# Optimization experiments

Measured on AMD Instinct MI355X. Metric: run time of the kernel, lower is better.

The kernel has to match this reference:

```python
import jax, jax.numpy as jnp
import numpy as np

# RT-DETR multi-scale deformable attention reference (PPMSDeformableAttention forward, value_mask=None)
SPATIAL_SHAPES = ((80, 80), (40, 40), (20, 20))  # (H, W) per level; sum(H*W) = 8400 = Len_v
NUM_HEADS = 8
NUM_LEVELS = 3
NUM_POINTS = 4


def _gather_corner(v_l, ix, iy, H, W):
    # v_l: [bs, heads, H*W, hd]; ix/iy: [bs, heads, N] int32 pixel indices (possibly out of range)
    valid = (ix >= 0) & (ix < W) & (iy >= 0) & (iy < H)
    idx = jnp.clip(iy, 0, H - 1) * W + jnp.clip(ix, 0, W - 1)
    g = jnp.take_along_axis(v_l, idx[..., None], axis=2)  # [bs, heads, N, hd]
    return jnp.where(valid[..., None], g, jnp.zeros((), v_l.dtype))


def _bilinear_sample(v_l, px, py, H, W):
    # grid_sample(align_corners=False, padding_mode='zeros') semantics.
    # v_l: [bs, heads, H*W, hd]; px/py: [bs, heads, N] continuous pixel coords
    x0 = jnp.floor(px).astype(jnp.int32)
    y0 = jnp.floor(py).astype(jnp.int32)
    x1, y1 = x0 + 1, y0 + 1
    wx1 = px - x0.astype(px.dtype)
    wy1 = py - y0.astype(py.dtype)
    wx0, wy0 = 1.0 - wx1, 1.0 - wy1
    out = (_gather_corner(v_l, x0, y0, H, W) * (wx0 * wy0)[..., None]
           + _gather_corner(v_l, x1, y0, H, W) * (wx1 * wy0)[..., None]
           + _gather_corner(v_l, x0, y1, H, W) * (wx0 * wy1)[..., None]
           + _gather_corner(v_l, x1, y1, H, W) * (wx1 * wy1)[..., None])
    return out  # [bs, heads, N, hd]


def setup_inputs() -> dict:
    key = jax.random.key(0)
    ks = jax.random.split(key, 8)
    bs, Lq, C = 32, 300, 256
    Lv = sum(h * w for h, w in SPATIAL_SHAPES)
    tp = NUM_HEADS * NUM_LEVELS * NUM_POINTS  # 96
    s = 1.0 / np.sqrt(C)
    return {
        "query": jax.random.normal(ks[0], (bs, Lq, C), jnp.float32),
        "reference_points": jax.random.uniform(ks[1], (bs, Lq, NUM_LEVELS, 4), jnp.float32, 0.05, 0.95),
        "value": jax.random.normal(ks[2], (bs, Lv, C), jnp.float32),
        "Wv": jax.random.normal(ks[3], (C, C), jnp.float32) * s,
        "bv": jnp.zeros((C,), jnp.float32),
        "Woff": jax.random.normal(ks[4], (C, tp * 2), jnp.float32) * (s * 0.1),
        "boff": jax.random.normal(ks[5], (tp * 2,), jnp.float32) * 0.5,
        "Watt": jax.random.normal(ks[6], (C, tp), jnp.float32) * s,
        "batt": jnp.zeros((tp,), jnp.float32),
        "Wout": jax.random.normal(ks[7], (C, C), jnp.float32) * s,
        "bout": jnp.zeros((C,), jnp.float32),
    }


def reference(query, reference_points, value, Wv, bv, Woff, boff, Watt, batt, Wout, bout):
    bs, Lq, C = query.shape
    H_, L, P = NUM_HEADS, NUM_LEVELS, NUM_POINTS
    hd = C // H_
    Lv = value.shape[1]

    # value projection -> [bs, heads, Lv, hd]
    v = (value @ Wv + bv).reshape(bs, Lv, H_, hd).transpose(0, 2, 1, 3)

    # sampling offsets and attention weights from query
    off = (query @ Woff + boff).reshape(bs, Lq, H_, L, P, 2)
    attw = jax.nn.softmax((query @ Watt + batt).reshape(bs, Lq, H_, L * P), axis=-1)
    attw = attw.reshape(bs, Lq, H_, L, P)

    # reference_points last dim == 4: (cx, cy, w, h) normalized
    ref_xy = reference_points[:, :, None, :, None, :2]  # [bs,Lq,1,L,1,2]
    ref_wh = reference_points[:, :, None, :, None, 2:]
    loc = ref_xy + off / P * ref_wh * 0.5  # [bs,Lq,H,L,P,2], normalized [0,1]

    out = jnp.zeros((bs, Lq, H_, hd), query.dtype)
    start = 0
    for l, (H, W) in enumerate(SPATIAL_SHAPES):
        v_l = v[:, :, start:start + H * W]  # [bs, heads, H*W, hd]
        start += H * W
        # normalized -> pixel coords (align_corners=False): p = loc * size - 0.5
        locl = loc[:, :, :, l]  # [bs, Lq, heads, P, 2]
        px = locl[..., 0] * W - 0.5
        py = locl[..., 1] * H - 0.5
        # [bs, Lq, heads, P] -> [bs, heads, Lq*P]
        px = px.transpose(0, 2, 1, 3).reshape(bs, H_, Lq * P)
        py = py.transpose(0, 2, 1, 3).reshape(bs, H_, Lq * P)
        sampled = _bilinear_sample(v_l, px, py, H, W)  # [bs, heads, Lq*P, hd]
        sampled = sampled.reshape(bs, H_, Lq, P, hd)
        out = out + jnp.einsum('bhqpd,bqhp->bqhd', sampled, attw[:, :, :, l])

    out = out.reshape(bs, Lq, C)
    return out @ Wout + bout
```

## Files before the change

### kernel.cpp

```cpp
#include <hip/hip_runtime.h>
#include <hip/hip_bf16.h>

#define BS 32
#define LQ 300
#define CDIM 256
#define HEADS 8
#define HD 32
#define NLEVELS 3
#define NPOINTS 4
#define LV 8400
#define NOA 288

typedef __attribute__((ext_vector_type(4))) float f32x4;
typedef __attribute__((ext_vector_type(8))) short short8;
typedef __attribute__((ext_vector_type(8))) unsigned short u16x8;
typedef __attribute__((ext_vector_type(4))) unsigned short u16x4;

__device__ __forceinline__ unsigned short f2bf(float f) {
    __hip_bfloat16 h = __float2bfloat16(f);
    return __bfloat16_as_ushort(h);
}
__device__ __forceinline__ float bf2f(unsigned short u) {
    union { unsigned u; float f; } v; v.u = ((unsigned)u) << 16;
    return v.f;
}

__global__ void prep_weights_kernel(
    const float* __restrict__ Wv, const float* __restrict__ Wout,
    const float* __restrict__ Woff, const float* __restrict__ Watt,
    unsigned short* __restrict__ WvT, unsigned short* __restrict__ WoutT,
    unsigned short* __restrict__ WoaT)
{
    const int bid = blockIdx.x;
    const int k = threadIdx.x;
    if (bid < 256) {
        WvT[bid * 256 + k] = f2bf(Wv[k * 256 + bid]);
    } else if (bid < 512) {
        const int n = bid - 256;
        WoutT[n * 256 + k] = f2bf(Wout[k * 256 + n]);
    } else {
        const int n = bid - 512;
        const float w = (n < 192) ? Woff[k * 192 + n] : Watt[k * 96 + (n - 192)];
        WoaT[n * 256 + k] = f2bf(w);
    }
}

#define BM 128
#define BK 32
#define PAD 40
#define EPAD 264
#define NT (CDIM / BK)

__global__ __launch_bounds__(512) void proj_value_mfma(
    const float* __restrict__ value, const unsigned short* __restrict__ WvT,
    const float* __restrict__ bv, unsigned short* __restrict__ vout)
{
    __shared__ alignas(16) unsigned short lds_w[2][256 * PAD];
    __shared__ alignas(16) unsigned short lds_x[2][128 * PAD];
    unsigned short* lds_ep = &lds_w[0][0];

    const int tid = threadIdx.x;
    const int lane = tid & 63;
    const int wave = tid >> 6;
    const int wm = wave >> 2;
    const int wn = wave & 3;
    const long row0 = (long)blockIdx.x * BM;

    const int wr = tid >> 1, wk = (tid & 1) * 16;
    const unsigned short* wptr = WvT + (size_t)wr * CDIM + wk;
    const int xr = tid >> 2, xk = (tid & 3) * 8;
    const float* xptr = value + (row0 + xr) * CDIM + xk;

    u16x8 wA0, wA1, wB0, wB1;
    f32x4 xA0, xA1, xB0, xB1;

#define LOADSET(s, kb) do {                                   \
        const u16x8* qw_ = (const u16x8*)(wptr + (kb));       \
        w##s##0 = qw_[0]; w##s##1 = qw_[1];                   \
        const float* p_ = xptr + (kb);                        \
        x##s##0 = *(const f32x4*)(p_);                        \
        x##s##1 = *(const f32x4*)(p_ + 4);                    \
    } while (0)

#define WRITESET(s, buf) do {                                 \
        u16x8* ww_ = (u16x8*)&lds_w[buf][wr * PAD + wk];      \
        ww_[0] = w##s##0; ww_[1] = w##s##1;                   \
        u16x8 t_;                                             \
        t_[0] = f2bf(x##s##0[0]); t_[1] = f2bf(x##s##0[1]);   \
        t_[2] = f2bf(x##s##0[2]); t_[3] = f2bf(x##s##0[3]);   \
        t_[4] = f2bf(x##s##1[0]); t_[5] = f2bf(x##s##1[1]);   \
        t_[6] = f2bf(x##s##1[2]); t_[7] = f2bf(x##s##1[3]);   \
        *(u16x8*)&lds_x[buf][xr * PAD + xk] = t_;             \
    } while (0)

    f32x4 acc[4][4] = {};
    const int la = lane & 15;
    const int lg = lane >> 4;

#define COMPUTE(buf) do {                                                     \
        const unsigned short* pw_ = &lds_w[buf][(wn * 64 + la) * PAD + lg * 8];\
        const unsigned short* px_ = &lds_x[buf][(wm * 64 + la) * PAD + lg * 8];\
        short8 xf_[4];                                                        \
        _Pragma("unroll")                                                     \
        for (int mf = 0; mf < 4; ++mf)                                        \
            xf_[mf] = *(const short8*)(px_ + mf * 16 * PAD);                  \
        _Pragma("unroll")                                                     \
        for (int nf = 0; nf < 4; ++nf) {                                      \
            const short8 wf_ = *(const short8*)(pw_ + nf * 16 * PAD);         \
            _Pragma("unroll")                                                 \
            for (int mf = 0; mf < 4; ++mf)                                    \
                acc[nf][mf] = __builtin_amdgcn_mfma_f32_16x16x32_bf16(        \
                    wf_, xf_[mf], acc[nf][mf], 0, 0, 0);                      \
        }                                                                     \
    } while (0)

    LOADSET(A, 0);
    LOADSET(B, BK);
    WRITESET(A, 0);
    __syncthreads();

#pragma unroll
    for (int t = 0; t < NT; t += 2) {
        WRITESET(B, 1);
        if (t + 2 < NT) LOADSET(A, (t + 2) * BK);
        COMPUTE(0);
        __syncthreads();
        if (t + 2 < NT) WRITESET(A, 0);
        if (t + 3 < NT) LOADSET(B, (t + 3) * BK);
        COMPUTE(1);
        __syncthreads();
    }

#pragma unroll
    for (int pass = 0; pass < 2; ++pass) {
        __syncthreads();
        if (wm == pass) {
#pragma unroll
            for (int nf = 0; nf < 4; ++nf) {
                const int nbase = wn * 64 + nf * 16 + lg * 4;
                const f32x4 bb = *(const f32x4*)&bv[nbase];
#pragma unroll
                for (int mf = 0; mf < 4; ++mf) {
                    const int mloc = mf * 16 + la;
                    u16x4 o;
#pragma unroll
                    for (int j = 0; j < 4; ++j) o[j] = f2bf(acc[nf][mf][j] + bb[j]);
                    *(u16x4*)&lds_ep[mloc * EPAD + nbase] = o;
                }
            }
        }
        __syncthreads();
        const int er = tid >> 3;
        const int ec = (tid & 7) * 32;
        const long gr = row0 + pass * 64 + er;
        const u16x8* src = (const u16x8*)&lds_ep[er * EPAD + ec];
        u16x8* dst = (u16x8*)&vout[gr * CDIM + ec];
#pragma unroll
        for (int i = 0; i < 4; ++i) dst[i] = src[i];
    }
#undef LOADSET
#undef WRITESET
#undef COMPUTE
}

#define APAD 40
#define BPAD 40

__global__ __launch_bounds__(256) void offatt_gemm_mfma(
    const float* __restrict__ query, const unsigned short* __restrict__ WoaT,
    const float* __restrict__ boff, const float* __restrict__ batt,
    float* __restrict__ offatt)
{
    __shared__ unsigned short lds_a[2][BM * APAD];
    __shared__ unsigned short lds_b[2][NOA * BPAD];

    const int tid = threadIdx.x;
    const int lane = tid & 63;
    const int wave = tid >> 6;
    const int wm = wave >> 1;
    const int wn = wave & 1;
    const long row0 = (long)blockIdx.x * BM;

    const int ar = tid >> 1;
    const int ak = (tid & 1) * 16;
    const float* aptr = query + (row0 + ar) * CDIM + ak;
    const unsigned short* bptr  = WoaT + (size_t)tid * CDIM;
    const unsigned short* bptr2 = WoaT + (size_t)(256 + tid) * CDIM;
    const bool extra = tid < 32;

    f32x4 arg[4];
    u16x8 brg[4], brg2[4];

    auto load_tile = [&](int kb) {
        const float* p = aptr + kb;
        arg[0] = *(const f32x4*)(p);
        arg[1] = *(const f32x4*)(p + 4);
        arg[2] = *(const f32x4*)(p + 8);
        arg[3] = *(const f32x4*)(p + 12);
        const u16x8* q = (const u16x8*)(bptr + kb);
        brg[0] = q[0]; brg[1] = q[1]; brg[2] = q[2]; brg[3] = q[3];
        if (extra) {
            const u16x8* q2 = (const u16x8*)(bptr2 + kb);
            brg2[0] = q2[0]; brg2[1] = q2[1]; brg2[2] = q2[2]; brg2[3] = q2[3];
        }
    };
    auto write_tile = [&](int buf) {
        u16x8 t0, t1;
#pragma unroll
        for (int i = 0; i < 4; ++i) {
            t0[i]     = f2bf(arg[0][i]);
            t0[i + 4] = f2bf(arg[1][i]);
            t1[i]     = f2bf(arg[2][i]);
            t1[i + 4] = f2bf(arg[3][i]);
        }
        u16x8* wa = (u16x8*)&lds_a[buf][ar * APAD + ak];
        wa[0] = t0; wa[1] = t1;
        u16x8* wb = (u16x8*)&lds_b[buf][tid * BPAD];
        wb[0] = brg[0]; wb[1] = brg[1]; wb[2] = brg[2]; wb[3] = brg[3];
        if (extra) {
            u16x8* wb2 = (u16x8*)&lds_b[buf][(256 + tid) * BPAD];
            wb2[0] = brg2[0]; wb2[1] = brg2[1]; wb2[2] = brg2[2]; wb2[3] = brg2[3];
        }
    };

    f32x4 acc[4][9] = {};
    const int la = lane & 15;
    const int lg = lane >> 4;

    load_tile(0);
    write_tile(0);
    __syncthreads();
    int cur = 0;

    for (int t = 0; t < CDIM / BK; ++t) {
        if (t + 1 < CDIM / BK) load_tile((t + 1) * BK);

        const unsigned short* pa = &lds_a[cur][(wm * 64 + la) * APAD + lg * 8];
        const unsigned short* pb = &lds_b[cur][(wn * 144 + la) * BPAD + lg * 8];
        short8 af[4];
#pragma unroll
        for (int mi = 0; mi < 4; ++mi)
            af[mi] = *(const short8*)(pa + mi * 16 * APAD);
#pragma unroll
        for (int ni = 0; ni < 9; ++ni) {
            const short8 bf = *(const short8*)(pb + ni * 16 * BPAD);
#pragma unroll
            for (int mi = 0; mi < 4; ++mi)
                acc[mi][ni] = __builtin_amdgcn_mfma_f32_16x16x32_bf16(af[mi], bf, acc[mi][ni], 0, 0, 0);
        }

        if (t + 1 < CDIM / BK) write_tile(cur ^ 1);
        __syncthreads();
        cur ^= 1;
    }

    float bias[9];
#pragma unroll
    for (int ni = 0; ni < 9; ++ni) {
        const int col = wn * 144 + ni * 16 + la;
        bias[ni] = (col < 192) ? boff[col] : batt[col - 192];
    }
#pragma unroll
    for (int mi = 0; mi < 4; ++mi) {
#pragma unroll
        for (int ni = 0; ni < 9; ++ni) {
            const int col = wn * 144 + ni * 16 + la;
#pragma unroll
            for (int j = 0; j < 4; ++j) {
                const long r = row0 + wm * 64 + mi * 16 + lg * 4 + j;
                offatt[r * NOA + col] = acc[mi][ni][j] + bias[ni];
            }
        }
    }
}

__global__ __launch_bounds__(256) void sample_kernel(
    const float* __restrict__ offatt, const float* __restrict__ refpts,
    const unsigned short* __restrict__ v, unsigned short* __restrict__ mid)
{
    __shared__ float oa_s[NOA];
    __shared__ float aw_s[96];
    __shared__ float px_s[96];
    __shared__ float py_s[96];

    const int tid = threadIdx.x;
    const int b = blockIdx.x / LQ;
    const int q = blockIdx.x % LQ;
    const long bq = (long)b * LQ + q;

    oa_s[tid] = offatt[bq * NOA + tid];
    if (tid < 32) oa_s[256 + tid] = offatt[bq * NOA + 256 + tid];
    __syncthreads();

    if (tid < 8) {
        float m = -1e30f;
#pragma unroll
        for (int i = 0; i < 12; ++i) m = fmaxf(m, oa_s[192 + tid * 12 + i]);
        float e[12];
        float s = 0.f;
#pragma unroll
        for (int i = 0; i < 12; ++i) { e[i] = __expf(oa_s[192 + tid * 12 + i] - m); s += e[i]; }
        const float inv = 1.f / s;
#pragma unroll
        for (int i = 0; i < 12; ++i) aw_s[tid * 12 + i] = e[i] * inv;
    }
    if (tid >= 128 && tid < 224) {
        const int t = tid - 128;
        const int h = t / 12, idx = t % 12, l = idx >> 2, p = idx & 3;
        const float* rp = refpts + (bq * NLEVELS + l) * 4;
        const float rx = rp[0], ry = rp[1], rw = rp[2], rh = rp[3];
        const float ox = oa_s[((h * NLEVELS + l) * NPOINTS + p) * 2 + 0];
        const float oy = oa_s[((h * NLEVELS + l) * NPOINTS + p) * 2 + 1];
        const float lx = rx + ox * 0.125f * rw;
        const float ly = ry + oy * 0.125f * rh;
        const int Wl = 80 >> l;
        px_s[t] = lx * (float)Wl - 0.5f;
        py_s[t] = ly * (float)Wl - 0.5f;
    }
    __syncthreads();

    const int h = tid >> 5;
    const int pg = (tid >> 3) & 3;
    const int d4 = tid & 7;
    const unsigned short* vb = v + ((size_t)b * LV) * CDIM + h * HD + d4 * 4;

    float a0 = 0.f, a1 = 0.f, a2 = 0.f, a3 = 0.f;
#pragma unroll
    for (int j = 0; j < 3; ++j) {
        const int i = pg * 3 + j;
        const int l = i >> 2;
        const int idx = h * 12 + i;
        const float px = px_s[idx], py = py_s[idx], aw = aw_s[idx];
        const int Wl = 80 >> l;
        const int start = (l == 0) ? 0 : (l == 1) ? 6400 : 8000;

        const float fx = floorf(px), fy = floorf(py);
        const int x0 = (int)fx, y0 = (int)fy;
        const float wx1 = px - fx, wy1 = py - fy;
        const float wx0 = 1.f - wx1, wy0 = 1.f - wy1;
        const float w00 = wx0 * wy0 * aw, w10 = wx1 * wy0 * aw;
        const float w01 = wx0 * wy1 * aw, w11 = wx1 * wy1 * aw;
        const bool x0v = (unsigned)x0 < (unsigned)Wl;
        const bool x1v = (unsigned)(x0 + 1) < (unsigned)Wl;
        const bool y0v = (unsigned)y0 < (unsigned)Wl;
        const bool y1v = (unsigned)(y0 + 1) < (unsigned)Wl;

        const unsigned short* base = vb + (size_t)start * CDIM;
        if (y0v) {
            const unsigned short* r0p = base + (size_t)(y0 * Wl) * CDIM;
            if (x0v) {
                const u16x4 u = *(const u16x4*)(r0p + (size_t)x0 * CDIM);
                a0 = fmaf(w00, bf2f(u[0]), a0); a1 = fmaf(w00, bf2f(u[1]), a1);
                a2 = fmaf(w00, bf2f(u[2]), a2); a3 = fmaf(w00, bf2f(u[3]), a3);
            }
            if (x1v) {
                const u16x4 u = *(const u16x4*)(r0p + (size_t)(x0 + 1) * CDIM);
                a0 = fmaf(w10, bf2f(u[0]), a0); a1 = fmaf(w10, bf2f(u[1]), a1);
                a2 = fmaf(w10, bf2f(u[2]), a2); a3 = fmaf(w10, bf2f(u[3]), a3);
            }
        }
        if (y1v) {
            const unsigned short* r1p = base + (size_t)((y0 + 1) * Wl) * CDIM;
            if (x0v) {
                const u16x4 u = *(const u16x4*)(r1p + (size_t)x0 * CDIM);
                a0 = fmaf(w01, bf2f(u[0]), a0); a1 = fmaf(w01, bf2f(u[1]), a1);
                a2 = fmaf(w01, bf2f(u[2]), a2); a3 = fmaf(w01, bf2f(u[3]), a3);
            }
            if (x1v) {
                const u16x4 u = *(const u16x4*)(r1p + (size_t)(x0 + 1) * CDIM);
                a0 = fmaf(w11, bf2f(u[0]), a0); a1 = fmaf(w11, bf2f(u[1]), a1);
                a2 = fmaf(w11, bf2f(u[2]), a2); a3 = fmaf(w11, bf2f(u[3]), a3);
            }
        }
    }

    a0 += __shfl_xor(a0, 8);  a1 += __shfl_xor(a1, 8);
    a2 += __shfl_xor(a2, 8);  a3 += __shfl_xor(a3, 8);
    a0 += __shfl_xor(a0, 16); a1 += __shfl_xor(a1, 16);
    a2 += __shfl_xor(a2, 16); a3 += __shfl_xor(a3, 16);

    if (pg == 0) {
        u16x4 o;
        o[0] = f2bf(a0); o[1] = f2bf(a1); o[2] = f2bf(a2); o[3] = f2bf(a3);
        *(u16x4*)&mid[bq * CDIM + h * HD + d4 * 4] = o;
    }
}

__global__ __launch_bounds__(256) void out_gemm_mfma(
    const unsigned short* __restrict__ mid, const unsigned short* __restrict__ WoutT,
    const float* __restrict__ bout, float* __restrict__ out)
{
    __shared__ unsigned short lds_w[2][256 * APAD];
    __shared__ unsigned short lds_x[2][BM * BPAD];

    const int tid = threadIdx.x;
    const int lane = tid & 63;
    const int wave = tid >> 6;
    const int wn = wave & 1;
    const int wm = wave >> 1;
    const long row0 = (long)blockIdx.x * BM;

    const unsigned short* wptr = WoutT + (size_t)tid * CDIM;
    const int xr = tid >> 1;
    const int xk = (tid & 1) * 16;
    const unsigned short* xptr = mid + (row0 + xr) * CDIM + xk;

    u16x8 wrg[4];
    u16x8 xrg[2];

    auto load_tile = [&](int kb) {
        const u16x8* qw = (const u16x8*)(wptr + kb);
        wrg[0] = qw[0]; wrg[1] = qw[1]; wrg[2] = qw[2]; wrg[3] = qw[3];
        const u16x8* qx = (const u16x8*)(xptr + kb);
        xrg[0] = qx[0]; xrg[1] = qx[1];
    };
    auto write_tile = [&](int buf) {
        u16x8* ww = (u16x8*)&lds_w[buf][tid * APAD];
        ww[0] = wrg[0]; ww[1] = wrg[1]; ww[2] = wrg[2]; ww[3] = wrg[3];
        u16x8* wx = (u16x8*)&lds_x[buf][xr * BPAD + xk];
        wx[0] = xrg[0]; wx[1] = xrg[1];
    };

    f32x4 acc[8][4] = {};
    const int la = lane & 15;
    const int lg = lane >> 4;

    load_tile(0);
    write_tile(0);
    __syncthreads();
    int cur = 0;

    for (int t = 0; t < CDIM / BK; ++t) {
        if (t + 1 < CDIM / BK) load_tile((t + 1) * BK);

        const unsigned short* pw = &lds_w[cur][(wn * 128 + la) * APAD + lg * 8];
        const unsigned short* px = &lds_x[cur][(wm * 64 + la) * BPAD + lg * 8];
        short8 xf[4];
#pragma unroll
        for (int mf = 0; mf < 4; ++mf)
            xf[mf] = *(const short8*)(px + mf * 16 * BPAD);
#pragma unroll
        for (int nf = 0; nf < 8; ++nf) {
            const short8 wf = *(const short8*)(pw + nf * 16 * APAD);
#pragma unroll
            for (int mf = 0; mf < 4; ++mf)
                acc[nf][mf] = __builtin_amdgcn_mfma_f32_16x16x32_bf16(wf, xf[mf], acc[nf][mf], 0, 0, 0);
        }

        if (t + 1 < CDIM / BK) write_tile(cur ^ 1);
        __syncthreads();
        cur ^= 1;
    }

#pragma unroll
    for (int nf = 0; nf < 8; ++nf) {
        const int nbase = wn * 128 + nf * 16 + lg * 4;
        const f32x4 bb = *(const f32x4*)&bout[nbase];
#pragma unroll
        for (int mf = 0; mf < 4; ++mf) {
            const long m = row0 + wm * 64 + mf * 16 + la;
            f32x4 o;
#pragma unroll
            for (int j = 0; j < 4; ++j) o[j] = acc[nf][mf][j] + bb[j];
            *(f32x4*)&out[m * CDIM + nbase] = o;
        }
    }
}

extern "C" void kernel_launch(void* const* d_in, const int* in_sizes, int n_in,
                              void* d_out, int out_size, void* d_ws, size_t ws_size,
                              hipStream_t stream) {
    const float* query = (const float*)d_in[0];
    const float* refp  = (const float*)d_in[1];
    const float* value = (const float*)d_in[2];
    const float* Wv    = (const float*)d_in[3];
    const float* bv    = (const float*)d_in[4];
    const float* Woff  = (const float*)d_in[5];
    const float* boff  = (const float*)d_in[6];
    const float* Watt  = (const float*)d_in[7];
    const float* batt  = (const float*)d_in[8];
    const float* Wout  = (const float*)d_in[9];
    const float* bout  = (const float*)d_in[10];
    float* out = (float*)d_out;

    char* ws = (char*)d_ws;
    unsigned short* v = (unsigned short*)ws;
    size_t off = (size_t)BS * LV * CDIM * 2;
    float* offatt = (float*)(ws + off);
    off += (size_t)BS * LQ * NOA * 4;
    unsigned short* mid = (unsigned short*)(ws + off);
    off += (size_t)BS * LQ * CDIM * 2;
    unsigned short* WvT = (unsigned short*)(ws + off);
    off += 256 * 256 * 2;
    unsigned short* WoaT = (unsigned short*)(ws + off);
    off += NOA * 256 * 2;
    unsigned short* WoutT = (unsigned short*)(ws + off);

    prep_weights_kernel<<<800, 256, 0, stream>>>(Wv, Wout, Woff, Watt, WvT, WoutT, WoaT);
    proj_value_mfma<<<(BS * LV) / BM, 512, 0, stream>>>(value, WvT, bv, v);
    offatt_gemm_mfma<<<(BS * LQ) / BM, 256, 0, stream>>>(query, WoaT, boff, batt, offatt);
    sample_kernel<<<BS * LQ, 256, 0, stream>>>(offatt, refp, v, mid);
    out_gemm_mfma<<<(BS * LQ) / BM, 256, 0, stream>>>(mid, WoutT, bout, out);
}
```

Before: 202.7 us.

## Load value-projection MFMA fragments directly from global memory, bypassing LDS staging

The value projection GEMM no longer stages the weight and input tiles through double-buffered LDS. Each wave now loads its own MFMA fragments straight from global memory into registers, converts fp32 to bf16 in registers, and keeps two register sets to overlap loads with compute. This removes the LDS writes, LDS reads and block barriers in the main loop. In exchange, inputs shared by several waves are fetched redundantly from global/L2, register pressure rises, and the per-lane global accesses are strided.

```diff
diff --git a/kernel.cpp b/kernel.cpp
--- a/kernel.cpp
+++ b/kernel.cpp
@@ -23,6 +23,12 @@
 __device__ __forceinline__ float bf2f(unsigned short u) {
     union { unsigned u; float f; } v; v.u = ((unsigned)u) << 16;
     return v.f;
+}
+__device__ __forceinline__ short8 cvt8(const f32x4 a, const f32x4 b) {
+    u16x8 c;
+#pragma unroll
+    for (int i = 0; i < 4; ++i) { c[i] = f2bf(a[i]); c[i + 4] = f2bf(b[i]); }
+    union { u16x8 u; short8 s; } v; v.u = c; return v.s;
 }
 
 __global__ void prep_weights_kernel(
@@ -47,7 +53,6 @@
 
 #define BM 128
 #define BK 32
-#define PAD 40
 #define EPAD 264
 #define NT (CDIM / BK)
 
@@ -55,9 +60,7 @@
     const float* __restrict__ value, const unsigned short* __restrict__ WvT,
     const float* __restrict__ bv, unsigned short* __restrict__ vout)
 {
-    __shared__ alignas(16) unsigned short lds_w[2][256 * PAD];
-    __shared__ alignas(16) unsigned short lds_x[2][128 * PAD];
-    unsigned short* lds_ep = &lds_w[0][0];
+    __shared__ alignas(16) unsigned short lds_ep[64 * EPAD];
 
     const int tid = threadIdx.x;
     const int lane = tid & 63;
@@ -65,75 +68,57 @@
     const int wm = wave >> 2;
     const int wn = wave & 3;
     const long row0 = (long)blockIdx.x * BM;
-
-    const int wr = tid >> 1, wk = (tid & 1) * 16;
-    const unsigned short* wptr = WvT + (size_t)wr * CDIM + wk;
-    const int xr = tid >> 2, xk = (tid & 3) * 8;
-    const float* xptr = value + (row0 + xr) * CDIM + xk;
-
-    u16x8 wA0, wA1, wB0, wB1;
-    f32x4 xA0, xA1, xB0, xB1;
-
-#define LOADSET(s, kb) do {                                   \
-        const u16x8* qw_ = (const u16x8*)(wptr + (kb));       \
-        w##s##0 = qw_[0]; w##s##1 = qw_[1];                   \
-        const float* p_ = xptr + (kb);                        \
-        x##s##0 = *(const f32x4*)(p_);                        \
-        x##s##1 = *(const f32x4*)(p_ + 4);                    \
-    } while (0)
-
-#define WRITESET(s, buf) do {                                 \
-        u16x8* ww_ = (u16x8*)&lds_w[buf][wr * PAD + wk];      \
-        ww_[0] = w##s##0; ww_[1] = w##s##1;                   \
-        u16x8 t_;                                             \
-        t_[0] = f2bf(x##s##0[0]); t_[1] = f2bf(x##s##0[1]);   \
-        t_[2] = f2bf(x##s##0[2]); t_[3] = f2bf(x##s##0[3]);   \
-        t_[4] = f2bf(x##s##1[0]); t_[5] = f2bf(x##s##1[1]);   \
-        t_[6] = f2bf(x##s##1[2]); t_[7] = f2bf(x##s##1[3]);   \
-        *(u16x8*)&lds_x[buf][xr * PAD + xk] = t_;             \
-    } while (0)
-
-    f32x4 acc[4][4] = {};
     const int la = lane & 15;
     const int lg = lane >> 4;
 
-#define COMPUTE(buf) do {                                                     \
-        const unsigned short* pw_ = &lds_w[buf][(wn * 64 + la) * PAD + lg * 8];\
-        const unsigned short* px_ = &lds_x[buf][(wm * 64 + la) * PAD + lg * 8];\
-        short8 xf_[4];                                                        \
-        _Pragma("unroll")                                                     \
-        for (int mf = 0; mf < 4; ++mf)                                        \
-            xf_[mf] = *(const short8*)(px_ + mf * 16 * PAD);                  \
-        _Pragma("unroll")                                                     \
-        for (int nf = 0; nf < 4; ++nf) {                                      \
-            const short8 wf_ = *(const short8*)(pw_ + nf * 16 * PAD);         \
-            _Pragma("unroll")                                                 \
-            for (int mf = 0; mf < 4; ++mf)                                    \
-                acc[nf][mf] = __builtin_amdgcn_mfma_f32_16x16x32_bf16(        \
-                    wf_, xf_[mf], acc[nf][mf], 0, 0, 0);                      \
-        }                                                                     \
+    const float* xbase = value + (row0 + wm * 64 + la) * (long)CDIM + lg * 8;
+    const unsigned short* wbase = WvT + (size_t)(wn * 64 + la) * CDIM + lg * 8;
+
+    f32x4 xA[4][2], xB[4][2];
+    short8 wA[4], wB[4];
+
+#define LOADSET(s, kb) do {                                        \
+        _Pragma("unroll")                                          \
+        for (int mf = 0; mf < 4; ++mf) {                           \
+            const float* p_ = xbase + mf * 16 * CDIM + (kb);       \
+            x##s[mf][0] = *(const f32x4*)(p_);                     \
+            x##s[mf][1] = *(const f32x4*)(p_ + 4);                 \
+        }                                                          \
+        _Pragma("unroll")                                          \
+        for (int nf = 0; nf < 4; ++nf)                             \
+            w##s[nf] = *(const short8*)(wbase + nf * 16 * CDIM + (kb)); \
+    } while (0)
+
+    f32x4 acc[4][4] = {};
+
+#define COMPUTE(s) do {                                            \
+        short8 xf_[4];                                             \
+        _Pragma("unroll")                                          \
+        for (int mf = 0; mf < 4; ++mf)                             \
+            xf_[mf] = cvt8(x##s[mf][0], x##s[mf][1]);              \
+        _Pragma("unroll")                                          \
+        for (int nf = 0; nf < 4; ++nf) {                           \
+            _Pragma("unroll")                                      \
+            for (int mf = 0; mf < 4; ++mf)                         \
+                acc[nf][mf] = __builtin_amdgcn_mfma_f32_16x16x32_bf16( \
+                    w##s[nf], xf_[mf], acc[nf][mf], 0, 0, 0);      \
+        }                                                          \
     } while (0)
 
     LOADSET(A, 0);
     LOADSET(B, BK);
-    WRITESET(A, 0);
-    __syncthreads();
 
 #pragma unroll
     for (int t = 0; t < NT; t += 2) {
-        WRITESET(B, 1);
+        COMPUTE(A);
         if (t + 2 < NT) LOADSET(A, (t + 2) * BK);
-        COMPUTE(0);
-        __syncthreads();
-        if (t + 2 < NT) WRITESET(A, 0);
+        COMPUTE(B);
         if (t + 3 < NT) LOADSET(B, (t + 3) * BK);
-        COMPUTE(1);
-        __syncthreads();
     }
 
 #pragma unroll
     for (int pass = 0; pass < 2; ++pass) {
-        __syncthreads();
+        if (pass) __syncthreads();
         if (wm == pass) {
 #pragma unroll
             for (int nf = 0; nf < 4; ++nf) {
@@ -159,7 +144,6 @@
         for (int i = 0; i < 4; ++i) dst[i] = src[i];
     }
 #undef LOADSET
-#undef WRITESET
 #undef COMPUTE
 }
 
```

After: 348.4 us. 71.9% more time.
